# Optimization experiments

Measured on AMD Instinct MI355X. Metric: run time of the kernel, lower is better.

Reference implementation:

```python
import jax, jax.numpy as jnp
import numpy as np

# ---- fixed architecture hyperparameters (match init_kwargs) ----
B, S = 4, 1024
L, H, DM, DF = 4, 8, 512, 2048
DH = DM // H          # 64 head dim (= 2*R after gated SPE filter)
NS = 5                # num_sines
R = 32                # num_realizations
M = 2 * DH            # favor_feature_dims = 128 (split as +/- of 64 projections)
LN_EPS = 1e-5
ATT_EPS = 1e-6


def layernorm(x, g, b):
    mu = x.mean(-1, keepdims=True)
    var = ((x - mu) ** 2).mean(-1, keepdims=True)
    return (x - mu) * jax.lax.rsqrt(var + LN_EPS) * g + b


def sine_spe(freqs, offsets, gains, noise, seq_len):
    """SineSPE positional code. freqs/offsets/gains: (H,DH,NS); noise: (H,DH,2NS,R).
    Returns qbar, kbar of shape (S,H,DH,R)."""
    pos = jnp.arange(seq_len, dtype=freqs.dtype)
    f = jax.nn.sigmoid(freqs)[:, :, None, :] / 2.0                       # (H,DH,1,NS)
    ph_q = 2.0 * jnp.pi * f * pos[None, None, :, None] + offsets[:, :, None, :]
    ph_k = 2.0 * jnp.pi * f * pos[None, None, :, None]
    om_q = jnp.stack([jnp.cos(ph_q), jnp.sin(ph_q)], -1).reshape(H, DH, seq_len, 2 * NS)
    om_k = jnp.stack([jnp.cos(ph_k), jnp.sin(ph_k)], -1).reshape(H, DH, seq_len, 2 * NS)
    g = jax.nn.softplus(gains)
    g = jnp.stack([g, g], -1).reshape(H, DH, 2 * NS)                      # upsample gains
    z = noise * g[..., None] / jnp.sqrt(jnp.asarray(2.0 * NS, freqs.dtype))
    qbar = jnp.einsum('hdsk,hdkr->shdr', om_q, z)
    kbar = jnp.einsum('hdsk,hdkr->shdr', om_k, z)
    scale = (R * DH) ** 0.25
    return qbar / scale, kbar / scale


def spe_filter(q, k, qbar, kbar, gate, gnoise):
    """Gated SPE filter. q,k: (B,S,H,DH); qbar/kbar: (S,H,DH,R); gate: (H,DH); gnoise: (H,DH,R).
    Returns qhat, khat of shape (B,S,H,2R)."""
    g = jax.nn.sigmoid(gate)[..., None]                                   # (H,DH,1)
    gn = gnoise / (DH * R) ** 0.25
    seq_len = qbar.shape[0]
    bias = jnp.broadcast_to(jnp.sqrt(g) * gn, (seq_len, H, DH, R))
    qb = jnp.concatenate([jnp.sqrt(1.0 - g) * qbar, bias], -1)            # (S,H,DH,2R)
    kb = jnp.concatenate([jnp.sqrt(1.0 - g) * kbar, bias], -1)
    qhat = jnp.einsum('bshd,shdr->bshr', q, qb)
    khat = jnp.einsum('bshd,shdr->bshr', k, kb)
    return qhat, khat


def favor(x, omega):
    """FAVOR+ softmax feature map. x: (B,S,H,DH); omega: (DH, M//2) -> (B,S,H,M)."""
    x = x * (DH ** -0.25)                                                 # sqrt(softmax_temp), temp=1/sqrt(DH)
    half_norm = 0.5 * jnp.sum(x * x, -1, keepdims=True)
    u = jnp.einsum('bshe,em->bshm', x, omega)
    phi = jnp.concatenate([jnp.exp(u - half_norm), jnp.exp(-u - half_norm)], -1)
    return phi / jnp.sqrt(jnp.asarray(M, x.dtype))


def causal_linear_attention(Q, K, V):
    """Causal linear (kernelized) attention via lax.scan. Q,K: (B,S,H,M); V: (B,S,H,DH)."""
    Bv = Q.shape[0]

    def step(carry, qkv):
        Skv, sk = carry
        q, k, v = qkv                                                     # (B,H,M),(B,H,M),(B,H,DH)
        Skv = Skv + jnp.einsum('bhm,bhd->bhmd', k, v)
        sk = sk + k
        num = jnp.einsum('bhm,bhmd->bhd', q, Skv)
        den = jnp.einsum('bhm,bhm->bh', q, sk) + ATT_EPS
        return (Skv, sk), num / den[..., None]

    init = (jnp.zeros((Bv, H, M, DH), Q.dtype), jnp.zeros((Bv, H, M), Q.dtype))
    xs = tuple(jnp.moveaxis(t, 1, 0) for t in (Q, K, V))
    _, out = jax.lax.scan(step, init, xs)
    return jnp.moveaxis(out, 0, 1)                                        # (B,S,H,DH)


def setup_inputs() -> dict:
    key = jax.random.key(0)
    ks = jax.random.split(key, 14)

    def rn(k, shape, scale=1.0):
        return jax.random.normal(k, shape, dtype=jnp.float32) * scale

    return {
        'x': rn(ks[0], (B, S, DM)),
        'Wq': rn(ks[1], (L, DM, DM), 0.02), 'bq': jnp.zeros((L, DM), jnp.float32),
        'Wk': rn(ks[2], (L, DM, DM), 0.02), 'bk': jnp.zeros((L, DM), jnp.float32),
        'Wv': rn(ks[3], (L, DM, DM), 0.02), 'bv': jnp.zeros((L, DM), jnp.float32),
        'Wo': rn(ks[4], (L, DM, DM), 0.02), 'bo': jnp.zeros((L, DM), jnp.float32),
        'W1': rn(ks[5], (L, DM, DF), 0.02), 'b1': jnp.zeros((L, DF), jnp.float32),
        'W2': rn(ks[6], (L, DF, DM), 0.02), 'b2': jnp.zeros((L, DM), jnp.float32),
        'ln1_g': jnp.ones((L, DM), jnp.float32), 'ln1_b': jnp.zeros((L, DM), jnp.float32),
        'ln2_g': jnp.ones((L, DM), jnp.float32), 'ln2_b': jnp.zeros((L, DM), jnp.float32),
        'spe_freqs': rn(ks[7], (L, H, DH, NS)),
        'spe_offsets': rn(ks[8], (L, H, DH, NS)),
        'spe_gains': rn(ks[9], (L, H, DH, NS)),
        'spe_noise': rn(ks[10], (L, H, DH, 2 * NS, R)),
        'gate': rn(ks[11], (L, H, DH)),
        'gate_noise': rn(ks[12], (L, H, DH, R)),
        'favor_omega': rn(ks[13], (L, DH, M // 2)),
    }


def reference(x, Wq, bq, Wk, bk, Wv, bv, Wo, bo, W1, b1, W2, b2,
              ln1_g, ln1_b, ln2_g, ln2_b,
              spe_freqs, spe_offsets, spe_gains, spe_noise, gate, gate_noise, favor_omega):
    Bv, Sv, _ = x.shape
    out = x
    for l in range(L):
        qbar, kbar = sine_spe(spe_freqs[l], spe_offsets[l], spe_gains[l], spe_noise[l], Sv)
        q = (out @ Wq[l] + bq[l]).reshape(Bv, Sv, H, DH)
        k = (out @ Wk[l] + bk[l]).reshape(Bv, Sv, H, DH)
        v = (out @ Wv[l] + bv[l]).reshape(Bv, Sv, H, DH)
        qh, kh = spe_filter(q, k, qbar, kbar, gate[l], gate_noise[l])
        Qf = favor(qh, favor_omega[l])
        Kf = favor(kh, favor_omega[l])
        att = causal_linear_attention(Qf, Kf, v).reshape(Bv, Sv, DM)
        att = att @ Wo[l] + bo[l]
        h = layernorm(out + att, ln1_g[l], ln1_b[l])
        y = jax.nn.relu(h @ W1[l] + b1[l]) @ W2[l] + b2[l]
        out = layernorm(h + y, ln2_g[l], ln2_b[l])
    return out
```

## Files before the change

kernel.cpp:

```cpp
#include <hip/hip_runtime.h>
#include <math.h>

#define BB 4
#define SS 1024
#define LL 4
#define HH 8
#define DM 512
#define DF 2048
#define DH 64
#define NS 5
#define RR 32
#define MM 128
#define NC 16
#define CHK 64
#define QKV_N 1536

#define INV_SQRT10   0.316227766016838f
#define INV_SCALE    0.148650889375340f
#define TEMP_SCALE   0.353553390593274f
#define INV_SQRT_M   0.088388347648318f
#define TWO_PI       6.283185307179586f

typedef __attribute__((ext_vector_type(8))) short bf16x8;
typedef __attribute__((ext_vector_type(4))) float f32x4;

__device__ __forceinline__ unsigned short f2bf(float f) {
  union { float f; unsigned int u; } v; v.f = f;
  unsigned int r = v.u + 0x7FFFu + ((v.u >> 16) & 1u);
  return (unsigned short)(r >> 16);
}

__device__ __forceinline__ float bf2f(unsigned short u) {
  union { unsigned int u; float f; } v; v.u = (unsigned int)u << 16;
  return v.f;
}

__device__ __forceinline__ void gld_lds16(const unsigned short* g, unsigned short* l) {
  __builtin_amdgcn_global_load_lds((const __attribute__((address_space(1))) void*)g,
                                   (__attribute__((address_space(3))) void*)l,
                                   16, 0, 0);
}

template<int RELU, int OUT_BF, int SPLITK>
__global__ __launch_bounds__(256)
void gemm_mfma_n64(const unsigned short* __restrict__ A, const unsigned short* __restrict__ Bt,
                   const float* __restrict__ bias, float* __restrict__ Cf,
                   unsigned short* __restrict__ Cbf, int M, int N, int K)
{
  __shared__ unsigned short As[128 * 32];
  __shared__ unsigned short Bs[64 * 32];
  const int tid  = threadIdx.x;
  const int w    = tid >> 6;
  const int lane = tid & 63;
  const int row0 = blockIdx.y * 128;
  const int col0 = blockIdx.x * 64;
  const int kz   = (SPLITK > 1) ? blockIdx.z : 0;
  const int Ks   = K / SPLITK;
  const int kbeg = kz * Ks;
  const int wr = (w >> 1) * 64;
  const int wc = (w & 1) * 32;
  const int c0 = w * 2, c1 = w * 2 + 1;
  const int m0 = c0 * 16 + (lane >> 2);
  const int m1 = c1 * 16 + (lane >> 2);
  const int mb = w * 16 + (lane >> 2);
  const int kA = (lane & 3) * 8;

  f32x4 acc[4][2] = {};

  for (int k0 = kbeg; k0 < kbeg + Ks; k0 += 32) {
    gld_lds16(&A [(size_t)(row0 + m0) * K + k0 + kA], &As[c0 * 512]);
    gld_lds16(&A [(size_t)(row0 + m1) * K + k0 + kA], &As[c1 * 512]);
    gld_lds16(&Bt[(size_t)(col0 + mb) * K + k0 + kA], &Bs[w * 512]);
    __syncthreads();
    const int rA = wr + (lane & 15);
    const int rB = wc + (lane & 15);
    const int kk = (lane >> 4) * 8;
    bf16x8 af[4], bfr[2];
#pragma unroll
    for (int i = 0; i < 4; ++i)
      af[i]  = *reinterpret_cast<const bf16x8*>(&As[(rA + i * 16) * 32 + kk]);
#pragma unroll
    for (int i = 0; i < 2; ++i)
      bfr[i] = *reinterpret_cast<const bf16x8*>(&Bs[(rB + i * 16) * 32 + kk]);
#pragma unroll
    for (int mi = 0; mi < 4; ++mi)
#pragma unroll
      for (int ni = 0; ni < 2; ++ni)
        acc[mi][ni] = __builtin_amdgcn_mfma_f32_16x16x32_bf16(af[mi], bfr[ni], acc[mi][ni], 0, 0, 0);
    __syncthreads();
  }
  const int cr = (lane >> 4) * 4;
  const int cc = lane & 15;
  float* Cfo = Cf + (size_t)kz * M * N;
#pragma unroll
  for (int mi = 0; mi < 4; ++mi) {
#pragma unroll
    for (int ni = 0; ni < 2; ++ni) {
      const int col = col0 + wc + ni * 16 + cc;
      const float bv = (kz == 0) ? bias[col] : 0.f;
#pragma unroll
      for (int r = 0; r < 4; ++r) {
        const int row = row0 + wr + mi * 16 + cr + r;
        float v = acc[mi][ni][r] + bv;
        if (RELU) v = fmaxf(v, 0.f);
        if (OUT_BF) Cbf[(size_t)row * N + col] = f2bf(v);
        else        Cfo[(size_t)row * N + col] = v;
      }
    }
  }
}

__global__ __launch_bounds__(256)
void transpose_bf(const float* __restrict__ W, unsigned short* __restrict__ Wt, int K, int N,
                  size_t inStride, size_t outStride)
{
  const float* Wl = W + blockIdx.z * inStride;
  unsigned short* Wtl = Wt + blockIdx.z * outStride;
  __shared__ float tile[32][33];
  const int k0 = blockIdx.y * 32, n0 = blockIdx.x * 32;
  const int tx = threadIdx.x & 31, ty = threadIdx.x >> 5;
#pragma unroll
  for (int j = 0; j < 4; ++j)
    tile[ty + 8 * j][tx] = Wl[(size_t)(k0 + ty + 8 * j) * N + n0 + tx];
  __syncthreads();
#pragma unroll
  for (int j = 0; j < 4; ++j)
    Wtl[(size_t)(n0 + ty + 8 * j) * K + k0 + tx] = f2bf(tile[tx][ty + 8 * j]);
}

__global__ __launch_bounds__(256)
void pack_bias(const float* __restrict__ bq, const float* __restrict__ bk,
               const float* __restrict__ bv, float* __restrict__ out)
{
  const int l = blockIdx.y;
  const int i = blockIdx.x * 256 + threadIdx.x;
  if (i < QKV_N)
    out[l * QKV_N + i] = (i < 512) ? bq[l * DM + i] : (i < 1024) ? bk[l * DM + i - 512]
                                                                 : bv[l * DM + i - 1024];
}

__global__ __launch_bounds__(256)
void cvt_bf16(const float* __restrict__ in, unsigned short* __restrict__ out, int n4)
{
  const int i = blockIdx.x * 256 + threadIdx.x;
  if (i < n4) {
    const float4 v = reinterpret_cast<const float4*>(in)[i];
    ushort4 o;
    o.x = f2bf(v.x); o.y = f2bf(v.y); o.z = f2bf(v.z); o.w = f2bf(v.w);
    reinterpret_cast<ushort4*>(out)[i] = o;
  }
}

__global__ __launch_bounds__(256)
void spe_prep_all(const float* __restrict__ gains, const float* __restrict__ noise,
                  const float* __restrict__ gate, const float* __restrict__ gnoise,
                  const float* __restrict__ offsets,
                  unsigned short* __restrict__ zpb, unsigned short* __restrict__ wbb,
                  float2* __restrict__ offcs)
{
  const int i = blockIdx.x * 256 + threadIdx.x;
  const int NZ = LL * HH * RR * 10 * DH;
  const int NW = LL * HH * RR * DH;
  const int NO = LL * HH * DH * NS;
  if (i < NZ) {
    const int d = i & 63;
    int j = i >> 6;
    const int k = j % 10; j /= 10;
    const int r = j & 31; j >>= 5;
    const int h = j & 7;  const int l = j >> 3;
    const int lhd = (l * HH + h) * DH + d;
    const float ga = gains[lhd * NS + (k >> 1)];
    const float sp = (ga > 20.f) ? ga : log1pf(__expf(ga));
    const float gg = 1.f / (1.f + __expf(-gate[lhd]));
    const float c1 = sqrtf(fmaxf(1.f - gg, 0.f));
    const float nz = noise[((size_t)lhd * 10 + k) * 32 + r];
    zpb[i] = f2bf(nz * sp * c1 * (INV_SQRT10 * INV_SCALE));
  } else if (i < NZ + NW) {
    int j = i - NZ;
    const int d = j & 63; j >>= 6;
    const int r = j & 31; j >>= 5;
    const int h = j & 7;  const int l = j >> 3;
    const int lhd = (l * HH + h) * DH + d;
    const float gg = 1.f / (1.f + __expf(-gate[lhd]));
    wbb[i - NZ] = f2bf(sqrtf(gg) * gnoise[(size_t)lhd * 32 + r] * INV_SCALE);
  } else if (i < NZ + NW + NO) {
    const int j = i - NZ - NW;
    float sn, cn;
    __sincosf(offsets[j], &sn, &cn);
    offcs[j] = make_float2(cn, sn);
  }
}

__global__ __launch_bounds__(256)
void spe_xhat(const float* __restrict__ freqs, const float2* __restrict__ offcs,
              const unsigned short* __restrict__ zpb, const unsigned short* __restrict__ wbb,
              const float* __restrict__ qkv, const unsigned short* __restrict__ omgT,
              unsigned short* __restrict__ QfKfB)
{
  const int s = blockIdx.x;
  const int h = blockIdx.y;
  const int t = threadIdx.x;
  const int w = t >> 6;
  const int lane = t & 63;
  __shared__ float omqT[10][64];
  __shared__ float omkT[10][64];
  __shared__ unsigned short qbT[64 * 64];
  __shared__ unsigned short kbT[64 * 64];
  __shared__ unsigned short rQ[16 * 64];
  __shared__ unsigned short rK[16 * 64];
  __shared__ float hqp[4][8];
  __shared__ float hnl[8];

  for (int e = t; e < DH * NS; e += 256) {
    const int d = e / NS, ns = e - d * NS;
    const float fr = 0.5f / (1.f + __expf(-freqs[(h * DH + d) * NS + ns]));
    float sn, cn;
    __sincosf(TWO_PI * fr * (float)s, &sn, &cn);
    const float2 oc = offcs[(h * DH + d) * NS + ns];
    omkT[2 * ns][d]     = cn;
    omkT[2 * ns + 1][d] = sn;
    omqT[2 * ns][d]     = cn * oc.x - sn * oc.y;
    omqT[2 * ns + 1][d] = sn * oc.x + cn * oc.y;
  }
  {
    const int b = t >> 6, d = t & 63;
    const size_t idx = ((size_t)b * SS + s) * QKV_N + h * DH + d;
    const int sd = d ^ ((b & 7) << 3);
    rQ[b * 64 + sd] = f2bf(qkv[idx] * TEMP_SCALE);
    rK[b * 64 + sd] = f2bf(qkv[idx + 512] * TEMP_SCALE);
  }
  for (int i = t; i < 768; i += 256) {
    rQ[256 + i] = 0;
    rK[256 + i] = 0;
  }
  __syncthreads();
  {
    const int r = t >> 3, dg = t & 7, d0 = dg * 8;
    float accq[8] = {}, acck[8] = {};
    const unsigned short* zr = zpb + (size_t)(h * RR + r) * 10 * 64 + d0;
#pragma unroll
    for (int k = 0; k < 10; ++k) {
      const bf16x8 zv = *reinterpret_cast<const bf16x8*>(zr + (size_t)k * 64);
      const float4 oq0 = *reinterpret_cast<const float4*>(&omqT[k][d0]);
      const float4 oq1 = *reinterpret_cast<const float4*>(&omqT[k][d0 + 4]);
      const float4 ok0 = *reinterpret_cast<const float4*>(&omkT[k][d0]);
      const float4 ok1 = *reinterpret_cast<const float4*>(&omkT[k][d0 + 4]);
      float zf[8];
#pragma unroll
      for (int j = 0; j < 8; ++j) zf[j] = bf2f((unsigned short)zv[j]);
      accq[0] += zf[0] * oq0.x; accq[1] += zf[1] * oq0.y;
      accq[2] += zf[2] * oq0.z; accq[3] += zf[3] * oq0.w;
      accq[4] += zf[4] * oq1.x; accq[5] += zf[5] * oq1.y;
      accq[6] += zf[6] * oq1.z; accq[7] += zf[7] * oq1.w;
      acck[0] += zf[0] * ok0.x; acck[1] += zf[1] * ok0.y;
      acck[2] += zf[2] * ok0.z; acck[3] += zf[3] * ok0.w;
      acck[4] += zf[4] * ok1.x; acck[5] += zf[5] * ok1.y;
      acck[6] += zf[6] * ok1.z; acck[7] += zf[7] * ok1.w;
    }
    bf16x8 qv, kv;
#pragma unroll
    for (int j = 0; j < 8; ++j) {
      qv[j] = (short)f2bf(accq[j]);
      kv[j] = (short)f2bf(acck[j]);
    }
    const int sd0 = d0 ^ ((r & 7) << 3);
    *reinterpret_cast<bf16x8*>(&qbT[r * 64 + sd0]) = qv;
    *reinterpret_cast<bf16x8*>(&kbT[r * 64 + sd0]) = kv;
    const bf16x8 wv = *reinterpret_cast<const bf16x8*>(&wbb[(size_t)(h * RR + r) * 64 + d0]);
    *reinterpret_cast<bf16x8*>(&qbT[(32 + r) * 64 + sd0]) = wv;
    *reinterpret_cast<bf16x8*>(&kbT[(32 + r) * 64 + sd0]) = wv;
  }
  __syncthreads();
  f32x4 aq = {0.f, 0.f, 0.f, 0.f}, ak = {0.f, 0.f, 0.f, 0.f};
  const int arow = lane & 15;
  const int colr = w * 16 + (lane & 15);
#pragma unroll
  for (int kt = 0; kt < 2; ++kt) {
    const int g = kt * 4 + (lane >> 4);
    const bf16x8 fAq = *reinterpret_cast<const bf16x8*>(&rQ[arow * 64 + ((g ^ (arow & 7)) << 3)]);
    const bf16x8 fAk = *reinterpret_cast<const bf16x8*>(&rK[arow * 64 + ((g ^ (arow & 7)) << 3)]);
    const bf16x8 fBq = *reinterpret_cast<const bf16x8*>(&qbT[colr * 64 + ((g ^ (colr & 7)) << 3)]);
    const bf16x8 fBk = *reinterpret_cast<const bf16x8*>(&kbT[colr * 64 + ((g ^ (colr & 7)) << 3)]);
    aq = __builtin_amdgcn_mfma_f32_16x16x32_bf16(fAq, fBq, aq, 0, 0, 0);
    ak = __builtin_amdgcn_mfma_f32_16x16x32_bf16(fAk, fBk, ak, 0, 0, 0);
  }
  float rq[4], rk2[4];
#pragma unroll
  for (int r = 0; r < 4; ++r) { rq[r] = aq[r] * aq[r]; rk2[r] = ak[r] * ak[r]; }
#pragma unroll
  for (int off = 1; off < 16; off <<= 1) {
#pragma unroll
    for (int r = 0; r < 4; ++r) {
      rq[r]  += __shfl_xor(rq[r],  off, 64);
      rk2[r] += __shfl_xor(rk2[r], off, 64);
    }
  }
  if (lane == 0) {
#pragma unroll
    for (int r = 0; r < 4; ++r) { hqp[w][r] = rq[r]; hqp[w][4 + r] = rk2[r]; }
  }
  __syncthreads();

  if (t < 8) {
    const int b = t & 3;
    const int ko = (t >> 2) * 4;
    hnl[t] = 0.5f * (hqp[0][ko + b] + hqp[1][ko + b] + hqp[2][ko + b] + hqp[3][ko + b]);
  }
  if (lane < 16) {
#pragma unroll
    for (int r = 0; r < 4; ++r) {
      const int d = w * 16 + lane;
      rQ[r * 64 + (d ^ (r << 3))] = f2bf(aq[r]);
      rK[r * 64 + (d ^ (r << 3))] = f2bf(ak[r]);
    }
  }
  __syncthreads();

  f32x4 uq = {0.f, 0.f, 0.f, 0.f}, uk = {0.f, 0.f, 0.f, 0.f};
  const int ocol = w * 16 + (lane & 15);
#pragma unroll
  for (int kt = 0; kt < 2; ++kt) {
    const int g = kt * 4 + (lane >> 4);
    const bf16x8 fAq = *reinterpret_cast<const bf16x8*>(&rQ[arow * 64 + ((g ^ (arow & 7)) << 3)]);
    const bf16x8 fAk = *reinterpret_cast<const bf16x8*>(&rK[arow * 64 + ((g ^ (arow & 7)) << 3)]);
    const bf16x8 fB  = *reinterpret_cast<const bf16x8*>(&omgT[(size_t)ocol * 64 + g * 8]);
    uq = __builtin_amdgcn_mfma_f32_16x16x32_bf16(fAq, fB, uq, 0, 0, 0);
    uk = __builtin_amdgcn_mfma_f32_16x16x32_bf16(fAk, fB, uk, 0, 0, 0);
  }
  if (lane < 16) {
#pragma unroll
    for (int r = 0; r < 4; ++r) {
      const size_t rowq = ((size_t)r * SS + s) * HH + h;
      const size_t rowk = rowq + (size_t)BB * SS * HH;
      const float hq = hnl[r], hk = hnl[4 + r];
      QfKfB[rowq * MM + ocol]      = f2bf(__expf( uq[r] - hq) * INV_SQRT_M);
      QfKfB[rowq * MM + ocol + 64] = f2bf(__expf(-uq[r] - hq) * INV_SQRT_M);
      QfKfB[rowk * MM + ocol]      = f2bf(__expf( uk[r] - hk) * INV_SQRT_M);
      QfKfB[rowk * MM + ocol + 64] = f2bf(__expf(-uk[r] - hk) * INV_SQRT_M);
    }
  }
}

__global__ __launch_bounds__(256)
void attn_chunk_sums(const unsigned short* __restrict__ KfB, const float* __restrict__ qkv,
                     float* __restrict__ Sch, float* __restrict__ kch)
{
  const int c = blockIdx.x, h = blockIdx.y, b = blockIdx.z;
  const int tid = threadIdx.x;
  const int w = tid >> 6, lane = tid & 63;
  __shared__ unsigned short KcT[128 * 64];
  __shared__ unsigned short VT[64 * 64];
  const size_t srow0 = (size_t)b * SS + c * CHK;

  for (int i = tid; i < 8192; i += 256) {
    const int m = i & 127, t = i >> 7;
    KcT[m * 64 + (t ^ ((m & 7) << 3))] = KfB[((srow0 + t) * HH + h) * MM + m];
  }
  for (int i = tid; i < 4096; i += 256) {
    const int d = i & 63, tt = i >> 6;
    VT[d * 64 + (tt ^ ((d & 7) << 3))] = f2bf(qkv[(srow0 + tt) * QKV_N + 1024 + h * DH + d]);
  }
  __syncthreads();

  const int kk = (lane >> 4) * 8;
  f32x4 acc[2][4] = {};
#pragma unroll
  for (int kc = 0; kc < 2; ++kc) {
    const int k = kc * 32 + kk;
#pragma unroll
    for (int mi = 0; mi < 2; ++mi) {
      const int mA = w * 32 + mi * 16 + (lane & 15);
      const bf16x8 a = *reinterpret_cast<const bf16x8*>(&KcT[mA * 64 + (k ^ ((mA & 7) << 3))]);
#pragma unroll
      for (int ni = 0; ni < 4; ++ni) {
        const int dB = ni * 16 + (lane & 15);
        const bf16x8 bb = *reinterpret_cast<const bf16x8*>(&VT[dB * 64 + (k ^ ((dB & 7) << 3))]);
        acc[mi][ni] = __builtin_amdgcn_mfma_f32_16x16x32_bf16(a, bb, acc[mi][ni], 0, 0, 0);
      }
    }
  }
  const size_t base = (((size_t)b * HH + h) * NC + c);
  float* So = Sch + base * (MM * DH);
  const int cr = (lane >> 4) * 4, cc = lane & 15;
#pragma unroll
  for (int mi = 0; mi < 2; ++mi)
#pragma unroll
    for (int ni = 0; ni < 4; ++ni)
#pragma unroll
      for (int r = 0; r < 4; ++r)
        So[(size_t)(w * 32 + mi * 16 + cr + r) * DH + ni * 16 + cc] = acc[mi][ni][r];
  {
    const int m = tid >> 1, half = tid & 1;
    float ks = 0.f;
#pragma unroll
    for (int j = 0; j < 32; ++j) {
      const int t2 = half * 32 + j;
      ks += bf2f(KcT[m * 64 + (t2 ^ ((m & 7) << 3))]);
    }
    ks += __shfl_xor(ks, 1, 64);
    if (half == 0) kch[base * MM + m] = ks;
  }
}

__global__ __launch_bounds__(256)
void attn_scan(float* __restrict__ Sch, float* __restrict__ kch)
{
  const int bh = blockIdx.x, part = blockIdx.y;
  const int t = threadIdx.x;
  float* base = Sch + (size_t)bh * NC * (MM * DH);
  for (int e = part * 1024 + t; e < (part + 1) * 1024; e += 256) {
    float run = 0.f;
#pragma unroll
    for (int c = 0; c < NC; ++c) {
      const float v = base[(size_t)c * (MM * DH) + e];
      base[(size_t)c * (MM * DH) + e] = run;
      run += v;
    }
  }
  if (part == 0 && t < MM) {
    float* kb2 = kch + (size_t)bh * NC * MM;
    float run = 0.f;
#pragma unroll
    for (int c = 0; c < NC; ++c) {
      const float v = kb2[c * MM + t];
      kb2[c * MM + t] = run;
      run += v;
    }
  }
}

__global__ __launch_bounds__(256)
void attn_out(const unsigned short* __restrict__ QfKfB, const float* __restrict__ qkv,
              const float* __restrict__ Sch, const float* __restrict__ kch,
              unsigned short* __restrict__ att)
{
  const int c = blockIdx.x, h = blockIdx.y, b = blockIdx.z;
  const int tid = threadIdx.x;
  const int w = tid >> 6;
  const int lane = tid & 63;
  __shared__ unsigned short Qc[64 * 128];
  __shared__ unsigned short Sb[64 * 64];
  __shared__ unsigned short KVU[12288];
  __shared__ float skp[MM];
  __shared__ float denl[64];

  unsigned short* Kc   = KVU;
  unsigned short* SpxT = KVU;
  unsigned short* VT   = KVU + 8192;

  const size_t srow0 = (size_t)b * SS + c * CHK;
  const unsigned short* Qg = QfKfB + (srow0 * HH + h) * MM;
  const unsigned short* Kg = Qg + (size_t)BB * SS * HH * MM;

  if (tid < MM) skp[tid] = kch[(((size_t)b * HH + h) * NC + c) * MM + tid];

  for (int i = tid; i < 1024; i += 256) {
    const int s2 = i >> 4, m8 = (i & 15) * 8;
    const int sw = m8 ^ ((s2 & 15) << 3);
    *reinterpret_cast<bf16x8*>(&Qc[s2 * 128 + sw]) =
        *reinterpret_cast<const bf16x8*>(&Qg[(size_t)s2 * (HH * MM) + m8]);
    *reinterpret_cast<bf16x8*>(&Kc[s2 * 128 + sw]) =
        *reinterpret_cast<const bf16x8*>(&Kg[(size_t)s2 * (HH * MM) + m8]);
  }
  for (int i = tid; i < 4096; i += 256) {
    const int d = i & 63, tt = i >> 6;
    const float v = qkv[(srow0 + tt) * QKV_N + 1024 + h * DH + d];
    VT[d * 64 + (tt ^ ((d & 7) << 3))] = f2bf(v);
  }
  __syncthreads();

  const int sA = w * 16 + (lane & 15);
  const int kk = (lane >> 4) * 8;
  f32x4 acc_s[4] = {};
#pragma unroll
  for (int kc = 0; kc < 4; ++kc) {
    const int k = kc * 32 + kk;
    const bf16x8 aq = *reinterpret_cast<const bf16x8*>(&Qc[sA * 128 + (k ^ ((sA & 15) << 3))]);
#pragma unroll
    for (int n = 0; n < 4; ++n) {
      const int tB = n * 16 + (lane & 15);
      const bf16x8 bq = *reinterpret_cast<const bf16x8*>(&Kc[tB * 128 + (k ^ ((tB & 15) << 3))]);
      acc_s[n] = __builtin_amdgcn_mfma_f32_16x16x32_bf16(aq, bq, acc_s[n], 0, 0, 0);
    }
  }
  __syncthreads();

  {
    const int g = lane >> 4;
    const int tcol = lane & 15;
    float dintra[4] = {0.f, 0.f, 0.f, 0.f};
#pragma unroll
    for (int r = 0; r < 4; ++r) {
      const int s = w * 16 + g * 4 + r;
#pragma unroll
      for (int n = 0; n < 4; ++n) {
        const int t2 = n * 16 + tcol;
        const float v = (t2 <= s) ? acc_s[n][r] : 0.f;
        dintra[r] += v;
        Sb[s * 64 + (t2 ^ ((s & 7) << 3))] = f2bf(v);
      }
    }
#pragma unroll
    for (int off = 1; off < 16; off <<= 1)
#pragma unroll
      for (int r = 0; r < 4; ++r) dintra[r] += __shfl_xor(dintra[r], off, 64);
    if (tcol == 0) {
#pragma unroll
      for (int r = 0; r < 4; ++r) denl[w * 16 + g * 4 + r] = dintra[r];
    }
  }
  {
    const float* Sp = Sch + (((size_t)b * HH + h) * NC + c) * (MM * DH);
    for (int i = tid; i < 8192; i += 256) {
      const int d = i & 63, m = i >> 6;
      SpxT[d * 128 + (m ^ ((d & 15) << 3))] = f2bf(Sp[(size_t)m * DH + d]);
    }
  }
  __syncthreads();

  f32x4 acc_o[4] = {};
#pragma unroll
  for (int kc = 0; kc < 2; ++kc) {
    const int k = kc * 32 + kk;
    const bf16x8 as = *reinterpret_cast<const bf16x8*>(&Sb[sA * 64 + (k ^ ((sA & 7) << 3))]);
#pragma unroll
    for (int n = 0; n < 4; ++n) {
      const int dB = n * 16 + (lane & 15);
      const bf16x8 bv = *reinterpret_cast<const bf16x8*>(&VT[dB * 64 + (k ^ ((dB & 7) << 3))]);
      acc_o[n] = __builtin_amdgcn_mfma_f32_16x16x32_bf16(as, bv, acc_o[n], 0, 0, 0);
    }
  }
#pragma unroll
  for (int kc = 0; kc < 4; ++kc) {
    const int k = kc * 32 + kk;
    const bf16x8 aq = *reinterpret_cast<const bf16x8*>(&Qc[sA * 128 + (k ^ ((sA & 15) << 3))]);
#pragma unroll
    for (int n = 0; n < 4; ++n) {
      const int dB = n * 16 + (lane & 15);
      const bf16x8 bs = *reinterpret_cast<const bf16x8*>(&SpxT[dB * 128 + (k ^ ((dB & 15) << 3))]);
      acc_o[n] = __builtin_amdgcn_mfma_f32_16x16x32_bf16(aq, bs, acc_o[n], 0, 0, 0);
    }
  }
  {
    const int s2 = tid >> 2, part = tid & 3;
    float p = 0.f;
#pragma unroll
    for (int j = 0; j < 32; ++j) {
      const int m = part * 32 + j;
      p += bf2f(Qc[s2 * 128 + (m ^ ((s2 & 15) << 3))]) * skp[m];
    }
    p += __shfl_xor(p, 1, 64);
    p += __shfl_xor(p, 2, 64);
    if (part == 0) denl[s2] += p + 1e-6f;
  }
  __syncthreads();

  {
    const int g = lane >> 4;
    const int dcol = lane & 15;
#pragma unroll
    for (int r = 0; r < 4; ++r) {
      const int s = w * 16 + g * 4 + r;
      const float dinv = 1.f / denl[s];
#pragma unroll
      for (int n = 0; n < 4; ++n)
        att[(srow0 + s) * DM + h * DH + n * 16 + dcol] = f2bf(acc_o[n][r] * dinv);
    }
  }
}

template<int WBF, int NSUM>
__global__ __launch_bounds__(256)
void add_ln(const float* __restrict__ a, const float* __restrict__ bres, size_t sstride,
            const float* __restrict__ g, const float* __restrict__ be,
            float* __restrict__ out, unsigned short* __restrict__ outbf)
{
  const int row = blockIdx.x;
  const int t = threadIdx.x;
  const size_t base = (size_t)row * DM;
  float x0 = a[base + t] + bres[base + t];
  float x1 = a[base + t + 256] + bres[base + t + 256];
  if (NSUM == 2) {
    x0 += bres[sstride + base + t];
    x1 += bres[sstride + base + t + 256];
  }
  __shared__ float red[8];
  float ssum = x0 + x1;
#pragma unroll
  for (int off = 32; off > 0; off >>= 1) ssum += __shfl_xor(ssum, off, 64);
  const int wid = t >> 6, lid = t & 63;
  if (lid == 0) red[wid] = ssum;
  __syncthreads();
  const float mu = (red[0] + red[1] + red[2] + red[3]) * (1.f / DM);
  const float d0 = x0 - mu, d1 = x1 - mu;
  float sv = d0 * d0 + d1 * d1;
#pragma unroll
  for (int off = 32; off > 0; off >>= 1) sv += __shfl_xor(sv, off, 64);
  if (lid == 0) red[4 + wid] = sv;
  __syncthreads();
  const float var = (red[4] + red[5] + red[6] + red[7]) * (1.f / DM);
  const float rs = rsqrtf(var + 1e-5f);
  const float o0 = d0 * rs * g[t]       + be[t];
  const float o1 = d1 * rs * g[t + 256] + be[t + 256];
  out[base + t]       = o0;
  out[base + t + 256] = o1;
  if (WBF) {
    outbf[base + t]       = f2bf(o0);
    outbf[base + t + 256] = f2bf(o1);
  }
}

extern "C" void kernel_launch(void* const* d_in, const int* in_sizes, int n_in,
                              void* d_out, int out_size, void* d_ws, size_t ws_size,
                              hipStream_t stream)
{
  const float* x      = (const float*)d_in[0];
  const float* Wq     = (const float*)d_in[1];
  const float* bq     = (const float*)d_in[2];
  const float* Wk     = (const float*)d_in[3];
  const float* bk     = (const float*)d_in[4];
  const float* Wv     = (const float*)d_in[5];
  const float* bv     = (const float*)d_in[6];
  const float* Wo     = (const float*)d_in[7];
  const float* bo     = (const float*)d_in[8];
  const float* W1     = (const float*)d_in[9];
  const float* b1     = (const float*)d_in[10];
  const float* W2     = (const float*)d_in[11];
  const float* b2     = (const float*)d_in[12];
  const float* ln1g   = (const float*)d_in[13];
  const float* ln1b   = (const float*)d_in[14];
  const float* ln2g   = (const float*)d_in[15];
  const float* ln2b   = (const float*)d_in[16];
  const float* freqs  = (const float*)d_in[17];
  const float* offs   = (const float*)d_in[18];
  const float* gains  = (const float*)d_in[19];
  const float* noise  = (const float*)d_in[20];
  const float* gate   = (const float*)d_in[21];
  const float* gnoise = (const float*)d_in[22];
  const float* omega  = (const float*)d_in[23];

  float* ws = (float*)d_ws;
  size_t o = 0;
  float* curf = ws + o; o += (size_t)BB * SS * DM;
  float* qkvf = ws + o; o += (size_t)BB * SS * QKV_N;
  float* Sch  = ws + o; o += (size_t)BB * HH * NC * MM * DH;
  float* kch  = ws + o; o += (size_t)BB * HH * NC * MM;
  float* bqkv = ws + o; o += (size_t)LL * QKV_N;
  float2* offcs = (float2*)(ws + o); o += (size_t)LL * HH * DH * NS * 2;
  unsigned short* zpb = (unsigned short*)(ws + o); o += (size_t)LL * HH * RR * 10 * DH / 2;
  unsigned short* QfKfB = (unsigned short*)(ws + o); o += (size_t)2 * BB * SS * HH * MM / 2;
  unsigned short* attb  = (unsigned short*)(ws + o); o += (size_t)BB * SS * DM / 2;
  unsigned short* h_bf  = (unsigned short*)(ws + o); o += (size_t)BB * SS * DM / 2;
  unsigned short* curbf = (unsigned short*)(ws + o); o += (size_t)BB * SS * DM / 2;
  unsigned short* Wqkvt = (unsigned short*)(ws + o); o += (size_t)LL * QKV_N * DM / 2;
  unsigned short* Wot   = (unsigned short*)(ws + o); o += (size_t)LL * DM * DM / 2;
  unsigned short* W1t   = (unsigned short*)(ws + o); o += (size_t)LL * DF * DM / 2;
  unsigned short* W2t   = (unsigned short*)(ws + o); o += (size_t)LL * DM * DF / 2;
  unsigned short* omgT  = (unsigned short*)(ws + o); o += (size_t)LL * 4096 / 2;
  unsigned short* wbb   = (unsigned short*)(ws + o); o += (size_t)LL * HH * RR * DH / 2;

  const size_t SLICE = (size_t)BB * SS * DM;
  float* attp = qkvf;
  float* hbuf = qkvf + 2 * SLICE;
  float* ybuf = Sch;
  unsigned short* midbf = QfKfB;
  unsigned short* KfB   = QfKfB + (size_t)BB * SS * HH * MM;

  const int MROWS = BB * SS;

  cvt_bf16<<<(BB * SS * DM / 4 + 255) / 256, 256, 0, stream>>>(x, curbf, BB * SS * DM / 4);
  spe_prep_all<<<2856, 256, 0, stream>>>(gains, noise, gate, gnoise, offs, zpb, wbb, offcs);
  transpose_bf<<<dim3(16, 16, 4), 256, 0, stream>>>(Wq, Wqkvt,                     DM, DM, (size_t)DM * DM, (size_t)QKV_N * DM);
  transpose_bf<<<dim3(16, 16, 4), 256, 0, stream>>>(Wk, Wqkvt + (size_t)512 * DM,  DM, DM, (size_t)DM * DM, (size_t)QKV_N * DM);
  transpose_bf<<<dim3(16, 16, 4), 256, 0, stream>>>(Wv, Wqkvt + (size_t)1024 * DM, DM, DM, (size_t)DM * DM, (size_t)QKV_N * DM);
  transpose_bf<<<dim3(16, 16, 4), 256, 0, stream>>>(Wo, Wot, DM, DM, (size_t)DM * DM, (size_t)DM * DM);
  transpose_bf<<<dim3(64, 16, 4), 256, 0, stream>>>(W1, W1t, DM, DF, (size_t)DM * DF, (size_t)DF * DM);
  transpose_bf<<<dim3(16, 64, 4), 256, 0, stream>>>(W2, W2t, DF, DM, (size_t)DF * DM, (size_t)DM * DF);
  transpose_bf<<<dim3(2, 2, 4),   256, 0, stream>>>(omega, omgT, DH, MM / 2, (size_t)DH * (MM / 2), 4096);
  pack_bias<<<dim3(6, 4), 256, 0, stream>>>(bq, bk, bv, bqkv);

  for (int l = 0; l < LL; ++l) {
    const float* in = (l == 0) ? x : curf;

    gemm_mfma_n64<0, 0, 1><<<dim3(QKV_N / 64, MROWS / 128), 256, 0, stream>>>(
        curbf, Wqkvt + (size_t)l * QKV_N * DM, bqkv + (size_t)l * QKV_N,
        qkvf, (unsigned short*)nullptr, MROWS, QKV_N, DM);

    spe_xhat<<<dim3(SS, HH), 256, 0, stream>>>(
        freqs + (size_t)l * HH * DH * NS, offcs + (size_t)l * HH * DH * NS,
        zpb + (size_t)l * HH * RR * 10 * DH, wbb + (size_t)l * HH * RR * DH,
        qkvf, omgT + (size_t)l * 4096, QfKfB);

    attn_chunk_sums<<<dim3(NC, HH, BB), 256, 0, stream>>>(KfB, qkvf, Sch, kch);
    attn_scan<<<dim3(BB * HH, 8), 256, 0, stream>>>(Sch, kch);
    attn_out<<<dim3(NC, HH, BB), 256, 0, stream>>>(QfKfB, qkvf, Sch, kch, attb);

    gemm_mfma_n64<0, 0, 2><<<dim3(DM / 64, MROWS / 128, 2), 256, 0, stream>>>(
        attb, Wot + (size_t)l * DM * DM, bo + (size_t)l * DM,
        attp, (unsigned short*)nullptr, MROWS, DM, DM);

    add_ln<1, 2><<<MROWS, 256, 0, stream>>>(in, attp, SLICE,
        ln1g + (size_t)l * DM, ln1b + (size_t)l * DM, hbuf, h_bf);

    gemm_mfma_n64<1, 1, 1><<<dim3(DF / 64, MROWS / 128), 256, 0, stream>>>(
        h_bf, W1t + (size_t)l * DF * DM, b1 + (size_t)l * DF, (float*)nullptr, midbf, MROWS, DF, DM);

    gemm_mfma_n64<0, 0, 2><<<dim3(DM / 64, MROWS / 128, 2), 256, 0, stream>>>(
        midbf, W2t + (size_t)l * DM * DF, b2 + (size_t)l * DM,
        ybuf, (unsigned short*)nullptr, MROWS, DM, DF);

    if (l == LL - 1) {
      add_ln<0, 2><<<MROWS, 256, 0, stream>>>(hbuf, ybuf, SLICE,
          ln2g + (size_t)l * DM, ln2b + (size_t)l * DM, (float*)d_out, (unsigned short*)nullptr);
    } else {
      add_ln<1, 2><<<MROWS, 256, 0, stream>>>(hbuf, ybuf, SLICE,
          ln2g + (size_t)l * DM, ln2b + (size_t)l * DM, curf, curbf);
    }
  }
}
```

Before: 704.2 us.

## Store QKV projection as bf16 and fold temperature scale into SPE weights

```diff
diff --git a/kernel.cpp b/kernel.cpp
--- a/kernel.cpp
+++ b/kernel.cpp
@@ -174,7 +174,7 @@
     const float gg = 1.f / (1.f + __expf(-gate[lhd]));
     const float c1 = sqrtf(fmaxf(1.f - gg, 0.f));
     const float nz = noise[((size_t)lhd * 10 + k) * 32 + r];
-    zpb[i] = f2bf(nz * sp * c1 * (INV_SQRT10 * INV_SCALE));
+    zpb[i] = f2bf(nz * sp * c1 * (INV_SQRT10 * INV_SCALE * TEMP_SCALE));
   } else if (i < NZ + NW) {
     int j = i - NZ;
     const int d = j & 63; j >>= 6;
@@ -182,7 +182,7 @@
     const int h = j & 7;  const int l = j >> 3;
     const int lhd = (l * HH + h) * DH + d;
     const float gg = 1.f / (1.f + __expf(-gate[lhd]));
-    wbb[i - NZ] = f2bf(sqrtf(gg) * gnoise[(size_t)lhd * 32 + r] * INV_SCALE);
+    wbb[i - NZ] = f2bf(sqrtf(gg) * gnoise[(size_t)lhd * 32 + r] * (INV_SCALE * TEMP_SCALE));
   } else if (i < NZ + NW + NO) {
     const int j = i - NZ - NW;
     float sn, cn;
@@ -194,7 +194,7 @@
 __global__ __launch_bounds__(256)
 void spe_xhat(const float* __restrict__ freqs, const float2* __restrict__ offcs,
               const unsigned short* __restrict__ zpb, const unsigned short* __restrict__ wbb,
-              const float* __restrict__ qkv, const unsigned short* __restrict__ omgT,
+              const unsigned short* __restrict__ qkvb, const unsigned short* __restrict__ omgT,
               unsigned short* __restrict__ QfKfB)
 {
   const int s = blockIdx.x;
@@ -222,16 +222,18 @@
     omqT[2 * ns][d]     = cn * oc.x - sn * oc.y;
     omqT[2 * ns + 1][d] = sn * oc.x + cn * oc.y;
   }
-  {
-    const int b = t >> 6, d = t & 63;
-    const size_t idx = ((size_t)b * SS + s) * QKV_N + h * DH + d;
-    const int sd = d ^ ((b & 7) << 3);
-    rQ[b * 64 + sd] = f2bf(qkv[idx] * TEMP_SCALE);
-    rK[b * 64 + sd] = f2bf(qkv[idx + 512] * TEMP_SCALE);
-  }
-  for (int i = t; i < 768; i += 256) {
-    rQ[256 + i] = 0;
-    rK[256 + i] = 0;
+  if (t < 64) {
+    const int isK = t >> 5;
+    const int b = (t >> 3) & 3;
+    const int j = t & 7;
+    const unsigned short* src = qkvb + ((size_t)b * SS + s) * QKV_N + isK * 512 + h * DH + j * 8;
+    unsigned short* dst = (isK ? rK : rQ) + b * 64 + ((j ^ b) << 3);
+    *reinterpret_cast<bf16x8*>(dst) = *reinterpret_cast<const bf16x8*>(src);
+  } else if (t < 256) {
+    const int i = t - 64;
+    bf16x8 z = {};
+    if (i < 96) *reinterpret_cast<bf16x8*>(&rQ[256 + i * 8]) = z;
+    else        *reinterpret_cast<bf16x8*>(&rK[256 + (i - 96) * 8]) = z;
   }
   __syncthreads();
   {
@@ -342,7 +344,7 @@
 }
 
 __global__ __launch_bounds__(256)
-void attn_chunk_sums(const unsigned short* __restrict__ KfB, const float* __restrict__ qkv,
+void attn_chunk_sums(const unsigned short* __restrict__ KfB, const unsigned short* __restrict__ qkvb,
                      float* __restrict__ Sch, float* __restrict__ kch)
 {
   const int c = blockIdx.x, h = blockIdx.y, b = blockIdx.z;
@@ -356,9 +358,13 @@
     const int m = i & 127, t = i >> 7;
     KcT[m * 64 + (t ^ ((m & 7) << 3))] = KfB[((srow0 + t) * HH + h) * MM + m];
   }
-  for (int i = tid; i < 4096; i += 256) {
-    const int d = i & 63, tt = i >> 6;
-    VT[d * 64 + (tt ^ ((d & 7) << 3))] = f2bf(qkv[(srow0 + tt) * QKV_N + 1024 + h * DH + d]);
+  for (int i = tid; i < 512; i += 256) {
+    const int d = i & 63, oct = i >> 6;
+    const unsigned short* src = qkvb + (srow0 + oct * 8) * QKV_N + 1024 + h * DH + d;
+    bf16x8 v;
+#pragma unroll
+    for (int j = 0; j < 8; ++j) v[j] = (short)src[(size_t)j * QKV_N];
+    *reinterpret_cast<bf16x8*>(&VT[d * 64 + ((oct << 3) ^ ((d & 7) << 3))]) = v;
   }
   __syncthreads();
 
@@ -430,7 +436,7 @@
 }
 
 __global__ __launch_bounds__(256)
-void attn_out(const unsigned short* __restrict__ QfKfB, const float* __restrict__ qkv,
+void attn_out(const unsigned short* __restrict__ QfKfB, const unsigned short* __restrict__ qkvb,
               const float* __restrict__ Sch, const float* __restrict__ kch,
               unsigned short* __restrict__ att)
 {
@@ -462,10 +468,13 @@
     *reinterpret_cast<bf16x8*>(&Kc[s2 * 128 + sw]) =
         *reinterpret_cast<const bf16x8*>(&Kg[(size_t)s2 * (HH * MM) + m8]);
   }
-  for (int i = tid; i < 4096; i += 256) {
-    const int d = i & 63, tt = i >> 6;
-    const float v = qkv[(srow0 + tt) * QKV_N + 1024 + h * DH + d];
-    VT[d * 64 + (tt ^ ((d & 7) << 3))] = f2bf(v);
+  for (int i = tid; i < 512; i += 256) {
+    const int d = i & 63, oct = i >> 6;
+    const unsigned short* src = qkvb + (srow0 + oct * 8) * QKV_N + 1024 + h * DH + d;
+    bf16x8 v;
+#pragma unroll
+    for (int j = 0; j < 8; ++j) v[j] = (short)src[(size_t)j * QKV_N];
+    *reinterpret_cast<bf16x8*>(&VT[d * 64 + ((oct << 3) ^ ((d & 7) << 3))]) = v;
   }
   __syncthreads();
 
@@ -642,7 +651,7 @@
   float* ws = (float*)d_ws;
   size_t o = 0;
   float* curf = ws + o; o += (size_t)BB * SS * DM;
-  float* qkvf = ws + o; o += (size_t)BB * SS * QKV_N;
+  unsigned short* qkvb = (unsigned short*)(ws + o); o += (size_t)BB * SS * QKV_N / 2;
   float* Sch  = ws + o; o += (size_t)BB * HH * NC * MM * DH;
   float* kch  = ws + o; o += (size_t)BB * HH * NC * MM;
   float* bqkv = ws + o; o += (size_t)LL * QKV_N;
@@ -660,9 +669,9 @@
   unsigned short* wbb   = (unsigned short*)(ws + o); o += (size_t)LL * HH * RR * DH / 2;
 
   const size_t SLICE = (size_t)BB * SS * DM;
-  float* attp = qkvf;
-  float* hbuf = qkvf + 2 * SLICE;
+  float* attp = Sch;
   float* ybuf = Sch;
+  float* hbuf = (float*)qkvb;
   unsigned short* midbf = QfKfB;
   unsigned short* KfB   = QfKfB + (size_t)BB * SS * HH * MM;
 
@@ -682,18 +691,18 @@
   for (int l = 0; l < LL; ++l) {
     const float* in = (l == 0) ? x : curf;
 
-    gemm_mfma_n64<0, 0, 1><<<dim3(QKV_N / 64, MROWS / 128), 256, 0, stream>>>(
+    gemm_mfma_n64<0, 1, 1><<<dim3(QKV_N / 64, MROWS / 128), 256, 0, stream>>>(
         curbf, Wqkvt + (size_t)l * QKV_N * DM, bqkv + (size_t)l * QKV_N,
-        qkvf, (unsigned short*)nullptr, MROWS, QKV_N, DM);
+        (float*)nullptr, qkvb, MROWS, QKV_N, DM);
 
     spe_xhat<<<dim3(SS, HH), 256, 0, stream>>>(
         freqs + (size_t)l * HH * DH * NS, offcs + (size_t)l * HH * DH * NS,
         zpb + (size_t)l * HH * RR * 10 * DH, wbb + (size_t)l * HH * RR * DH,
-        qkvf, omgT + (size_t)l * 4096, QfKfB);
-
-    attn_chunk_sums<<<dim3(NC, HH, BB), 256, 0, stream>>>(KfB, qkvf, Sch, kch);
+        qkvb, omgT + (size_t)l * 4096, QfKfB);
+
+    attn_chunk_sums<<<dim3(NC, HH, BB), 256, 0, stream>>>(KfB, qkvb, Sch, kch);
     attn_scan<<<dim3(BB * HH, 8), 256, 0, stream>>>(Sch, kch);
-    attn_out<<<dim3(NC, HH, BB), 256, 0, stream>>>(QfKfB, qkvf, Sch, kch, attb);
+    attn_out<<<dim3(NC, HH, BB), 256, 0, stream>>>(QfKfB, qkvb, Sch, kch, attb);
 
     gemm_mfma_n64<0, 0, 2><<<dim3(DM / 64, MROWS / 128, 2), 256, 0, stream>>>(
         attb, Wot + (size_t)l * DM * DM, bo + (size_t)l * DM,
```

After: 694.4 us. No clear change (-1.4%).
